# Performance work log

Measured on AMD Instinct MI355X. Metric: run time of the kernel, lower is better.

## Reference

```python
import jax, jax.numpy as jnp
import numpy as np

D_Z = 1024
D_MODEL = 4096
EPS = 1e-5  # torch LayerNorm default
CLAMP = 3.0


def setup_inputs() -> dict:
    key = jax.random.key(0)
    k_z, k_w, k_b = jax.random.split(key, 3)
    z = jax.random.normal(k_z, (8, 2048, D_Z), dtype=jnp.float32)
    # LayerNorm params (gamma=1, beta=0 init in torch; keep learnable form)
    ln_gamma = jnp.ones((D_Z,), dtype=jnp.float32)
    ln_beta = jnp.zeros((D_Z,), dtype=jnp.float32)
    # Linear: torch default init U(-1/sqrt(d_z), 1/sqrt(d_z))
    bound = 1.0 / np.sqrt(D_Z)
    W = jax.random.uniform(k_w, (D_Z, D_MODEL), minval=-bound, maxval=bound, dtype=jnp.float32)
    b = jax.random.uniform(k_b, (D_MODEL,), minval=-bound, maxval=bound, dtype=jnp.float32)
    scale = jnp.ones((1,), dtype=jnp.float32)
    return {"z": z, "ln_gamma": ln_gamma, "ln_beta": ln_beta, "W": W, "b": b, "scale": scale}


def reference(z, ln_gamma, ln_beta, W, b, scale):
    # LayerNorm over last dim
    mu = jnp.mean(z, axis=-1, keepdims=True)
    var = jnp.mean(jnp.square(z - mu), axis=-1, keepdims=True)
    zn = (z - mu) * jax.lax.rsqrt(var + EPS) * ln_gamma + ln_beta
    # Linear -> scalar scale -> tanh clamp
    x = (jnp.einsum('bsd,dm->bsm', zn, W) + b) * scale
    return jnp.tanh(x / CLAMP) * CLAMP
```

## Files before the change

kernel.cpp:

```cpp
#include <hip/hip_runtime.h>

#define M_DIM 16384
#define K_DIM 1024
#define N_DIM 4096
#define T_TILES (K_DIM / 32)

typedef __bf16 bf16x8 __attribute__((ext_vector_type(8)));
typedef float f32x4 __attribute__((ext_vector_type(4)));

__device__ __forceinline__ unsigned short f2bf(float f) {
    union { float f; unsigned int i; } v; v.f = f;
    unsigned int r = v.i + 0x7fffu + ((v.i >> 16) & 1u);
    return (unsigned short)(r >> 16);
}
__device__ __forceinline__ unsigned int pack2(float lo, float hi) {
    return ((unsigned int)f2bf(lo)) | (((unsigned int)f2bf(hi)) << 16);
}

__global__ __launch_bounds__(256) void prep_kernel(
        const float* __restrict__ z,
        const float* __restrict__ gamma,
        const float* __restrict__ beta,
        unsigned short* __restrict__ zn,
        const float* __restrict__ W,
        unsigned short* __restrict__ Wt) {
    __shared__ float t[32][33];
    const int tid = threadIdx.x;
    if (blockIdx.x < M_DIM / 4) {
        const int wave = tid >> 6;
        const int lane = tid & 63;
        const size_t row = (size_t)blockIdx.x * 4 + wave;
        const float* zr = z + row * K_DIM;

        float4 x[4];
#pragma unroll
        for (int v = 0; v < 4; v++) x[v] = *(const float4*)(zr + v * 256 + lane * 4);

        float s = 0.f, ss = 0.f;
#pragma unroll
        for (int v = 0; v < 4; v++) {
            s  += x[v].x + x[v].y + x[v].z + x[v].w;
            ss += x[v].x * x[v].x + x[v].y * x[v].y + x[v].z * x[v].z + x[v].w * x[v].w;
        }
#pragma unroll
        for (int o = 32; o; o >>= 1) { s += __shfl_xor(s, o, 64); ss += __shfl_xor(ss, o, 64); }
        const float mean = s * (1.f / K_DIM);
        const float var = ss * (1.f / K_DIM) - mean * mean;
        const float rstd = rsqrtf(var + 1e-5f);

#pragma unroll
        for (int v = 0; v < 4; v++) {
            float4 g = *(const float4*)(gamma + v * 256 + lane * 4);
            float4 b = *(const float4*)(beta + v * 256 + lane * 4);
            float o0 = (x[v].x - mean) * rstd * g.x + b.x;
            float o1 = (x[v].y - mean) * rstd * g.y + b.y;
            float o2 = (x[v].z - mean) * rstd * g.z + b.z;
            float o3 = (x[v].w - mean) * rstd * g.w + b.w;
            uint2 q; q.x = pack2(o0, o1); q.y = pack2(o2, o3);
            *(uint2*)(zn + row * K_DIM + v * 256 + lane * 4) = q;
        }
    } else {
        const int bid = blockIdx.x - M_DIM / 4;
        const int tx = tid & 31, ty = tid >> 5;
        const int n0 = (bid & (N_DIM / 32 - 1)) * 32, k0 = (bid / (N_DIM / 32)) * 32;
#pragma unroll
        for (int j = 0; j < 32; j += 8)
            t[ty + j][tx] = W[(size_t)(k0 + ty + j) * N_DIM + n0 + tx];
        __syncthreads();
#pragma unroll
        for (int j = 0; j < 32; j += 8)
            Wt[(size_t)(n0 + ty + j) * K_DIM + k0 + tx] = f2bf(t[tx][ty + j]);
    }
}

__device__ __forceinline__ void async_copy16(const unsigned short* g, unsigned short* l) {
    __builtin_amdgcn_global_load_lds(
        (const __attribute__((address_space(1))) unsigned int*)g,
        (__attribute__((address_space(3))) unsigned int*)l,
        16, 0, 0);
}

__global__ __launch_bounds__(512, 2) void gemm_kernel(
        const unsigned short* __restrict__ A,
        const unsigned short* __restrict__ B,
        const float* __restrict__ bias,
        const float* __restrict__ scale,
        float* __restrict__ out) {
    __shared__ __align__(16) unsigned short As[4][256 * 32];
    __shared__ __align__(16) unsigned short Bs[4][256 * 32];

    const int tid = threadIdx.x;
    const int wave = tid >> 6, lane = tid & 63;
    const int wm = wave >> 2, wn = wave & 3;
    const int rl = lane & 15;
    const int kc = lane >> 4;
    const int swz = (rl >> 1) & 3;

    const int bid = blockIdx.y * gridDim.x + blockIdx.x;
    const int id2 = (bid & 7) * 128 + (bid >> 3);
    const int bm = id2 >> 4, bn = id2 & 15;

    const int r0 = tid >> 2;
    const int c0 = ((tid & 3) ^ ((tid >> 3) & 3)) << 3;
    const unsigned short* agA = A + (size_t)(bm * 256 + r0) * K_DIM + c0;
    const unsigned short* agB = B + (size_t)(bn * 256 + r0) * K_DIM + c0;
    const int ldsu = wave * 512;

#define STAGE_A(t_, s_) do { \
        const unsigned short* g_ = agA + (t_) * 32; \
        async_copy16(g_,                 &As[s_][ldsu]); \
        async_copy16(g_ + 128 * K_DIM,   &As[s_][4096 + ldsu]); } while (0)
#define STAGE_B(t_, s_) do { \
        const unsigned short* g_ = agB + (t_) * 32; \
        async_copy16(g_,                 &Bs[s_][ldsu]); \
        async_copy16(g_ + 128 * K_DIM,   &Bs[s_][4096 + ldsu]); } while (0)

    f32x4 acc[8][4] = {};
    bf16x8 a[4], b[4];

#define READ_A(s_, mh_) do { \
        const unsigned short* as_ = As[s_]; \
        _Pragma("unroll") \
        for (int mt_ = 0; mt_ < 4; ++mt_) \
            a[mt_] = *(const bf16x8*)&as_[(wm * 128 + (mh_) * 64 + mt_ * 16 + rl) * 32 + ((kc ^ swz) << 3)]; } while (0)
#define READ_B(s_) do { \
        const unsigned short* bs_ = Bs[s_]; \
        _Pragma("unroll") \
        for (int nt_ = 0; nt_ < 4; ++nt_) \
            b[nt_] = *(const bf16x8*)&bs_[(wn * 64 + nt_ * 16 + rl) * 32 + ((kc ^ swz) << 3)]; } while (0)
#define MFG(mh_) do { \
        _Pragma("unroll") \
        for (int mt_ = 0; mt_ < 4; ++mt_) \
        _Pragma("unroll") \
        for (int nt_ = 0; nt_ < 4; ++nt_) \
            acc[(mh_) * 4 + mt_][nt_] = __builtin_amdgcn_mfma_f32_16x16x32_bf16(a[mt_], b[nt_], acc[(mh_) * 4 + mt_][nt_], 0, 0, 0); } while (0)

    STAGE_A(0, 0); STAGE_B(0, 0);
    STAGE_A(1, 1); STAGE_B(1, 1);
    STAGE_A(2, 2); STAGE_B(2, 2);
    asm volatile("s_waitcnt vmcnt(8)" ::: "memory");
    __builtin_amdgcn_s_barrier();
    asm volatile("" ::: "memory");

#pragma unroll 4
    for (int t = 0; t < T_TILES; ++t) {
        const int s = t & 3, ss = (t + 3) & 3;

        READ_A(s, 0); READ_B(s);
        if (t + 3 < T_TILES) STAGE_A(t + 3, ss);
        asm volatile("" ::: "memory");
        __builtin_amdgcn_s_barrier();
        asm volatile("s_waitcnt lgkmcnt(0)" ::: "memory");
        __builtin_amdgcn_sched_barrier(0);
        __builtin_amdgcn_s_setprio(1);
        MFG(0);
        __builtin_amdgcn_s_setprio(0);
        asm volatile("" ::: "memory");
        __builtin_amdgcn_s_barrier();
        asm volatile("" ::: "memory");

        READ_A(s, 1);
        if (t + 3 < T_TILES) STAGE_B(t + 3, ss);
        asm volatile("" ::: "memory");
        __builtin_amdgcn_s_barrier();
        asm volatile("s_waitcnt lgkmcnt(0)" ::: "memory");
        __builtin_amdgcn_sched_barrier(0);
        __builtin_amdgcn_s_setprio(1);
        MFG(1);
        __builtin_amdgcn_s_setprio(0);
        if (t < T_TILES - 1) {
            if (t < T_TILES - 3)       asm volatile("s_waitcnt vmcnt(8)" ::: "memory");
            else if (t == T_TILES - 3) asm volatile("s_waitcnt vmcnt(4)" ::: "memory");
            else                       asm volatile("s_waitcnt vmcnt(0)" ::: "memory");
            __builtin_amdgcn_s_barrier();
            asm volatile("" ::: "memory");
        }
    }
#undef STAGE_A
#undef STAGE_B
#undef READ_A
#undef READ_B
#undef MFG

    const float mfac = scale[0] * 0.96179669392236f;
#pragma unroll
    for (int nt = 0; nt < 4; ++nt) {
        const int gcol = bn * 256 + wn * 64 + nt * 16 + rl;
        const float bv = bias[gcol];
#pragma unroll
        for (int mt = 0; mt < 8; ++mt) {
            const int rbase = bm * 256 + wm * 128 + mt * 16 + kc * 4;
#pragma unroll
            for (int r = 0; r < 4; ++r) {
                const int grow = rbase + r;
                float tv = (acc[mt][nt][r] + bv) * mfac;
                float e = __builtin_amdgcn_exp2f(tv);
                out[(size_t)grow * N_DIM + gcol] = 3.f - 6.f * __builtin_amdgcn_rcpf(e + 1.f);
            }
        }
    }
}

extern "C" void kernel_launch(void* const* d_in, const int* in_sizes, int n_in,
                              void* d_out, int out_size, void* d_ws, size_t ws_size,
                              hipStream_t stream) {
    const float* z     = (const float*)d_in[0];
    const float* gamma = (const float*)d_in[1];
    const float* beta  = (const float*)d_in[2];
    const float* W     = (const float*)d_in[3];
    const float* b     = (const float*)d_in[4];
    const float* scale = (const float*)d_in[5];
    float* out = (float*)d_out;

    unsigned short* zn = (unsigned short*)d_ws;
    unsigned short* Wt = zn + (size_t)M_DIM * K_DIM;

    prep_kernel<<<M_DIM / 4 + (N_DIM / 32) * (K_DIM / 32), 256, 0, stream>>>(z, gamma, beta, zn, W, Wt);
    gemm_kernel<<<dim3(N_DIM / 256, M_DIM / 256), 512, 0, stream>>>(zn, Wt, b, scale, out);
}
```

Measured before the change: 475.3 us.

## Shrink GEMM tile to 128x256 with triple-buffered LDS for higher occupancy

The GEMM block tile drops from 256x256 to 128x256. Per-wave accumulators go from 8x4 to 4x4 MFMA tiles, and the LDS pipeline goes from 4 stages to 3 with a prefetch distance of 2. The K-loop becomes a single simpler phase with one barrier per tile, and launch bounds now request 4 blocks per CU so more blocks can be resident and hide latency. In exchange, arithmetic intensity per block falls, so more global and L2 traffic is needed to re-read B, and the prefetch depth is shallower.

Measured after the change: 480.9 us. Within noise of the previous version (+1.2%).

```diff
diff --git a/kernel.cpp b/kernel.cpp
--- a/kernel.cpp
+++ b/kernel.cpp
@@ -80,14 +80,14 @@
         16, 0, 0);
 }
 
-__global__ __launch_bounds__(512, 2) void gemm_kernel(
+__global__ __launch_bounds__(512, 4) void gemm_kernel(
         const unsigned short* __restrict__ A,
         const unsigned short* __restrict__ B,
         const float* __restrict__ bias,
         const float* __restrict__ scale,
         float* __restrict__ out) {
-    __shared__ __align__(16) unsigned short As[4][256 * 32];
-    __shared__ __align__(16) unsigned short Bs[4][256 * 32];
+    __shared__ __align__(16) unsigned short As[3][128 * 32];
+    __shared__ __align__(16) unsigned short Bs[3][256 * 32];
 
     const int tid = threadIdx.x;
     const int wave = tid >> 6, lane = tid & 63;
@@ -97,90 +97,67 @@
     const int swz = (rl >> 1) & 3;
 
     const int bid = blockIdx.y * gridDim.x + blockIdx.x;
-    const int id2 = (bid & 7) * 128 + (bid >> 3);
+    const int id2 = (bid & 7) * 256 + (bid >> 3);
     const int bm = id2 >> 4, bn = id2 & 15;
 
     const int r0 = tid >> 2;
     const int c0 = ((tid & 3) ^ ((tid >> 3) & 3)) << 3;
-    const unsigned short* agA = A + (size_t)(bm * 256 + r0) * K_DIM + c0;
+    const unsigned short* agA = A + (size_t)(bm * 128 + r0) * K_DIM + c0;
     const unsigned short* agB = B + (size_t)(bn * 256 + r0) * K_DIM + c0;
     const int ldsu = wave * 512;
 
-#define STAGE_A(t_, s_) do { \
-        const unsigned short* g_ = agA + (t_) * 32; \
-        async_copy16(g_,                 &As[s_][ldsu]); \
-        async_copy16(g_ + 128 * K_DIM,   &As[s_][4096 + ldsu]); } while (0)
-#define STAGE_B(t_, s_) do { \
-        const unsigned short* g_ = agB + (t_) * 32; \
-        async_copy16(g_,                 &Bs[s_][ldsu]); \
-        async_copy16(g_ + 128 * K_DIM,   &Bs[s_][4096 + ldsu]); } while (0)
+#define STAGE(t_, s_) do { \
+        const unsigned short* gA_ = agA + (t_) * 32; \
+        const unsigned short* gB_ = agB + (t_) * 32; \
+        async_copy16(gA_,                 &As[s_][ldsu]); \
+        async_copy16(gB_,                 &Bs[s_][ldsu]); \
+        async_copy16(gB_ + 128 * K_DIM,   &Bs[s_][ldsu + 4096]); } while (0)
 
-    f32x4 acc[8][4] = {};
+    f32x4 acc[4][4] = {};
     bf16x8 a[4], b[4];
 
-#define READ_A(s_, mh_) do { \
+#define READ_A(s_) do { \
         const unsigned short* as_ = As[s_]; \
         _Pragma("unroll") \
         for (int mt_ = 0; mt_ < 4; ++mt_) \
-            a[mt_] = *(const bf16x8*)&as_[(wm * 128 + (mh_) * 64 + mt_ * 16 + rl) * 32 + ((kc ^ swz) << 3)]; } while (0)
+            a[mt_] = *(const bf16x8*)&as_[(wm * 64 + mt_ * 16 + rl) * 32 + ((kc ^ swz) << 3)]; } while (0)
 #define READ_B(s_) do { \
         const unsigned short* bs_ = Bs[s_]; \
         _Pragma("unroll") \
         for (int nt_ = 0; nt_ < 4; ++nt_) \
             b[nt_] = *(const bf16x8*)&bs_[(wn * 64 + nt_ * 16 + rl) * 32 + ((kc ^ swz) << 3)]; } while (0)
-#define MFG(mh_) do { \
-        _Pragma("unroll") \
-        for (int mt_ = 0; mt_ < 4; ++mt_) \
-        _Pragma("unroll") \
-        for (int nt_ = 0; nt_ < 4; ++nt_) \
-            acc[(mh_) * 4 + mt_][nt_] = __builtin_amdgcn_mfma_f32_16x16x32_bf16(a[mt_], b[nt_], acc[(mh_) * 4 + mt_][nt_], 0, 0, 0); } while (0)
 
-    STAGE_A(0, 0); STAGE_B(0, 0);
-    STAGE_A(1, 1); STAGE_B(1, 1);
-    STAGE_A(2, 2); STAGE_B(2, 2);
-    asm volatile("s_waitcnt vmcnt(8)" ::: "memory");
+    STAGE(0, 0);
+    STAGE(1, 1);
+    asm volatile("s_waitcnt vmcnt(3)" ::: "memory");
     __builtin_amdgcn_s_barrier();
     asm volatile("" ::: "memory");
 
-#pragma unroll 4
+#pragma unroll
     for (int t = 0; t < T_TILES; ++t) {
-        const int s = t & 3, ss = (t + 3) & 3;
+        const int s = t % 3;
 
-        READ_A(s, 0); READ_B(s);
-        if (t + 3 < T_TILES) STAGE_A(t + 3, ss);
-        asm volatile("" ::: "memory");
-        __builtin_amdgcn_s_barrier();
-        asm volatile("s_waitcnt lgkmcnt(0)" ::: "memory");
-        __builtin_amdgcn_sched_barrier(0);
+        if (t + 2 < T_TILES) STAGE(t + 2, (t + 2) % 3);
+        READ_A(s); READ_B(s);
+
         __builtin_amdgcn_s_setprio(1);
-        MFG(0);
+#pragma unroll
+        for (int mt = 0; mt < 4; ++mt)
+#pragma unroll
+            for (int nt = 0; nt < 4; ++nt)
+                acc[mt][nt] = __builtin_amdgcn_mfma_f32_16x16x32_bf16(a[mt], b[nt], acc[mt][nt], 0, 0, 0);
         __builtin_amdgcn_s_setprio(0);
-        asm volatile("" ::: "memory");
-        __builtin_amdgcn_s_barrier();
-        asm volatile("" ::: "memory");
 
-        READ_A(s, 1);
-        if (t + 3 < T_TILES) STAGE_B(t + 3, ss);
-        asm volatile("" ::: "memory");
-        __builtin_amdgcn_s_barrier();
-        asm volatile("s_waitcnt lgkmcnt(0)" ::: "memory");
-        __builtin_amdgcn_sched_barrier(0);
-        __builtin_amdgcn_s_setprio(1);
-        MFG(1);
-        __builtin_amdgcn_s_setprio(0);
+        if (t < T_TILES - 2)       asm volatile("s_waitcnt vmcnt(3)" ::: "memory");
+        else if (t == T_TILES - 2) asm volatile("s_waitcnt vmcnt(0)" ::: "memory");
         if (t < T_TILES - 1) {
-            if (t < T_TILES - 3)       asm volatile("s_waitcnt vmcnt(8)" ::: "memory");
-            else if (t == T_TILES - 3) asm volatile("s_waitcnt vmcnt(4)" ::: "memory");
-            else                       asm volatile("s_waitcnt vmcnt(0)" ::: "memory");
             __builtin_amdgcn_s_barrier();
             asm volatile("" ::: "memory");
         }
     }
-#undef STAGE_A
-#undef STAGE_B
+#undef STAGE
 #undef READ_A
 #undef READ_B
-#undef MFG
 
     const float mfac = scale[0] * 0.96179669392236f;
 #pragma unroll
@@ -188,8 +165,8 @@
         const int gcol = bn * 256 + wn * 64 + nt * 16 + rl;
         const float bv = bias[gcol];
 #pragma unroll
-        for (int mt = 0; mt < 8; ++mt) {
-            const int rbase = bm * 256 + wm * 128 + mt * 16 + kc * 4;
+        for (int mt = 0; mt < 4; ++mt) {
+            const int rbase = bm * 128 + wm * 64 + mt * 16 + kc * 4;
 #pragma unroll
             for (int r = 0; r < 4; ++r) {
                 const int grow = rbase + r;
@@ -216,5 +193,5 @@
     unsigned short* Wt = zn + (size_t)M_DIM * K_DIM;
 
     prep_kernel<<<M_DIM / 4 + (N_DIM / 32) * (K_DIM / 32), 256, 0, stream>>>(z, gamma, beta, zn, W, Wt);
-    gemm_kernel<<<dim3(N_DIM / 256, M_DIM / 256), 512, 0, stream>>>(zn, Wt, b, scale, out);
+    gemm_kernel<<<dim3(N_DIM / 256, M_DIM / 128), 512, 0, stream>>>(zn, Wt, b, scale, out);
 }
```

## Load A operand directly from global into registers, stage only B in LDS

Applied to the files above, without the earlier changes.

Removes the LDS staging buffer for A. Each wave now loads its A fragments straight from global memory into registers, double-buffered across tiles, while B stays in a 4-stage LDS pipeline with a prefetch depth of 2. The aim is to cut LDS traffic, LDS capacity use and the number of barriers per tile. In exchange, A reads become per-lane 16-byte strided global loads that are duplicated across the waves sharing the same rows, which adds more VGPR pressure. The waitcnt handling is also much looser, with no explicit vmcnt waits inside the loop.

New measurement: 658.7 us. +38.6%, slower.

```diff
diff --git a/kernel.cpp b/kernel.cpp
--- a/kernel.cpp
+++ b/kernel.cpp
@@ -86,7 +86,6 @@
         const float* __restrict__ bias,
         const float* __restrict__ scale,
         float* __restrict__ out) {
-    __shared__ __align__(16) unsigned short As[4][256 * 32];
     __shared__ __align__(16) unsigned short Bs[4][256 * 32];
 
     const int tid = threadIdx.x;
@@ -102,85 +101,68 @@
 
     const int r0 = tid >> 2;
     const int c0 = ((tid & 3) ^ ((tid >> 3) & 3)) << 3;
-    const unsigned short* agA = A + (size_t)(bm * 256 + r0) * K_DIM + c0;
     const unsigned short* agB = B + (size_t)(bn * 256 + r0) * K_DIM + c0;
     const int ldsu = wave * 512;
 
-#define STAGE_A(t_, s_) do { \
-        const unsigned short* g_ = agA + (t_) * 32; \
-        async_copy16(g_,                 &As[s_][ldsu]); \
-        async_copy16(g_ + 128 * K_DIM,   &As[s_][4096 + ldsu]); } while (0)
+    const unsigned short* aglA = A + (size_t)(bm * 256 + wm * 128 + rl) * K_DIM + kc * 8;
+
 #define STAGE_B(t_, s_) do { \
         const unsigned short* g_ = agB + (t_) * 32; \
         async_copy16(g_,                 &Bs[s_][ldsu]); \
         async_copy16(g_ + 128 * K_DIM,   &Bs[s_][4096 + ldsu]); } while (0)
 
-    f32x4 acc[8][4] = {};
-    bf16x8 a[4], b[4];
-
-#define READ_A(s_, mh_) do { \
-        const unsigned short* as_ = As[s_]; \
+#define LOAD_A4(dst_, t_, h_) do { \
         _Pragma("unroll") \
         for (int mt_ = 0; mt_ < 4; ++mt_) \
-            a[mt_] = *(const bf16x8*)&as_[(wm * 128 + (mh_) * 64 + mt_ * 16 + rl) * 32 + ((kc ^ swz) << 3)]; } while (0)
+            dst_[mt_] = *(const bf16x8*)(aglA + (size_t)((h_) * 64 + mt_ * 16) * K_DIM + (t_) * 32); } while (0)
+
 #define READ_B(s_) do { \
         const unsigned short* bs_ = Bs[s_]; \
         _Pragma("unroll") \
         for (int nt_ = 0; nt_ < 4; ++nt_) \
             b[nt_] = *(const bf16x8*)&bs_[(wn * 64 + nt_ * 16 + rl) * 32 + ((kc ^ swz) << 3)]; } while (0)
-#define MFG(mh_) do { \
+
+    f32x4 acc[8][4] = {};
+    bf16x8 aP[4], aQ[4], aH[4], b[4];
+
+#define BODY(t_, CUR_, NXT_) do { \
+        const int s_ = (t_) & 3; \
+        READ_B(s_); \
+        LOAD_A4(aH, (t_), 1); \
+        if ((t_) + 2 < T_TILES) STAGE_B((t_) + 2, ((t_) + 2) & 3); \
+        if ((t_) + 1 < T_TILES) LOAD_A4(NXT_, (t_) + 1, 0); \
+        __builtin_amdgcn_s_setprio(1); \
         _Pragma("unroll") \
         for (int mt_ = 0; mt_ < 4; ++mt_) \
         _Pragma("unroll") \
         for (int nt_ = 0; nt_ < 4; ++nt_) \
-            acc[(mh_) * 4 + mt_][nt_] = __builtin_amdgcn_mfma_f32_16x16x32_bf16(a[mt_], b[nt_], acc[(mh_) * 4 + mt_][nt_], 0, 0, 0); } while (0)
-
-    STAGE_A(0, 0); STAGE_B(0, 0);
-    STAGE_A(1, 1); STAGE_B(1, 1);
-    STAGE_A(2, 2); STAGE_B(2, 2);
-    asm volatile("s_waitcnt vmcnt(8)" ::: "memory");
+            acc[mt_][nt_] = __builtin_amdgcn_mfma_f32_16x16x32_bf16(CUR_[mt_], b[nt_], acc[mt_][nt_], 0, 0, 0); \
+        __builtin_amdgcn_s_setprio(0); \
+        __builtin_amdgcn_s_setprio(1); \
+        _Pragma("unroll") \
+        for (int mt_ = 0; mt_ < 4; ++mt_) \
+        _Pragma("unroll") \
+        for (int nt_ = 0; nt_ < 4; ++nt_) \
+            acc[4 + mt_][nt_] = __builtin_amdgcn_mfma_f32_16x16x32_bf16(aH[mt_], b[nt_], acc[4 + mt_][nt_], 0, 0, 0); \
+        __builtin_amdgcn_s_setprio(0); \
+        __builtin_amdgcn_s_barrier(); \
+        asm volatile("" ::: "memory"); } while (0)
+
+    STAGE_B(0, 0);
+    LOAD_A4(aP, 0, 0);
+    STAGE_B(1, 1);
+    asm volatile("s_waitcnt vmcnt(6)" ::: "memory");
     __builtin_amdgcn_s_barrier();
     asm volatile("" ::: "memory");
 
-#pragma unroll 4
-    for (int t = 0; t < T_TILES; ++t) {
-        const int s = t & 3, ss = (t + 3) & 3;
-
-        READ_A(s, 0); READ_B(s);
-        if (t + 3 < T_TILES) STAGE_A(t + 3, ss);
-        asm volatile("" ::: "memory");
-        __builtin_amdgcn_s_barrier();
-        asm volatile("s_waitcnt lgkmcnt(0)" ::: "memory");
-        __builtin_amdgcn_sched_barrier(0);
-        __builtin_amdgcn_s_setprio(1);
-        MFG(0);
-        __builtin_amdgcn_s_setprio(0);
-        asm volatile("" ::: "memory");
-        __builtin_amdgcn_s_barrier();
-        asm volatile("" ::: "memory");
-
-        READ_A(s, 1);
-        if (t + 3 < T_TILES) STAGE_B(t + 3, ss);
-        asm volatile("" ::: "memory");
-        __builtin_amdgcn_s_barrier();
-        asm volatile("s_waitcnt lgkmcnt(0)" ::: "memory");
-        __builtin_amdgcn_sched_barrier(0);
-        __builtin_amdgcn_s_setprio(1);
-        MFG(1);
-        __builtin_amdgcn_s_setprio(0);
-        if (t < T_TILES - 1) {
-            if (t < T_TILES - 3)       asm volatile("s_waitcnt vmcnt(8)" ::: "memory");
-            else if (t == T_TILES - 3) asm volatile("s_waitcnt vmcnt(4)" ::: "memory");
-            else                       asm volatile("s_waitcnt vmcnt(0)" ::: "memory");
-            __builtin_amdgcn_s_barrier();
-            asm volatile("" ::: "memory");
-        }
+    for (int tp = 0; tp < T_TILES / 2; ++tp) {
+        BODY(2 * tp,     aP, aQ);
+        BODY(2 * tp + 1, aQ, aP);
     }
-#undef STAGE_A
 #undef STAGE_B
-#undef READ_A
+#undef LOAD_A4
 #undef READ_B
-#undef MFG
+#undef BODY
 
     const float mfac = scale[0] * 0.96179669392236f;
 #pragma unroll
```
